# Kernel tuning notes

Measured on AMD Instinct MI355X. Metric: run time of the kernel, lower is better.

## Reference

```python
import jax, jax.numpy as jnp
import numpy as np

HIDDEN = 512
HEADS = 8


def setup_inputs() -> dict:
    key = jax.random.key(0)
    ks = jax.random.split(key, 7)
    B, S, D = 4, 2048, HIDDEN
    scale = 1.0 / np.sqrt(D)
    return {
        "src": jax.random.normal(ks[0], (B, S, D), dtype=jnp.float32),
        "Wq": jax.random.normal(ks[1], (D, D), dtype=jnp.float32) * scale,
        "bq": jax.random.normal(ks[2], (D,), dtype=jnp.float32) * 0.01,
        "Wk": jax.random.normal(ks[3], (D, D), dtype=jnp.float32) * scale,
        "bk": jax.random.normal(ks[4], (D,), dtype=jnp.float32) * 0.01,
        "Wv": jax.random.normal(ks[5], (D, D), dtype=jnp.float32) * scale,
        "bv": jax.random.normal(ks[6], (D,), dtype=jnp.float32) * 0.01,
    }


def reference(src, Wq, bq, Wk, bk, Wv, bv):
    B, S, D = src.shape
    H = HEADS
    hd = D // H
    # QKV projections -> [B, S, H, hd]
    q = (src @ Wq + bq).reshape(B, S, H, hd)
    k = (src @ Wk + bk).reshape(B, S, H, hd)
    v = (src @ Wv + bv).reshape(B, S, H, hd)
    # scores [B, H, S, S]; note: NO causal mask (matches original module)
    scores = jnp.einsum("bqhd,bkhd->bhqk", q, k) / jnp.sqrt(jnp.asarray(hd, src.dtype))
    attn = jax.nn.softmax(scores, axis=-1)
    out = jnp.einsum("bhqk,bkhd->bqhd", attn, v)
    return out.reshape(B, S, D)
```

## Files before the change

kernel.cpp:

```cpp
#include <hip/hip_runtime.h>

typedef __bf16 bf16;
typedef __bf16 bf16x8 __attribute__((ext_vector_type(8)));
typedef __bf16 bf16x4 __attribute__((ext_vector_type(4)));
typedef float f32x4 __attribute__((ext_vector_type(4)));
typedef float f32x16 __attribute__((ext_vector_type(16)));
typedef unsigned int u32;

#define QK_SCALE 0.1803368801111204f

__device__ __forceinline__ int rc16(int row, int g) {
    return row * 256 + ((g ^ (row & 15)) << 4);
}
__device__ __forceinline__ int swzb(int row, int col) {
    return (((row) << 7) + ((col) << 1)) ^ (((row) & 7) << 4);
}

__device__ __forceinline__ void gload_lds16(const void* g, void* l) {
    __builtin_amdgcn_global_load_lds(
        (const __attribute__((address_space(1))) unsigned int*)g,
        (__attribute__((address_space(3))) unsigned int*)l, 16, 0, 0);
}

__device__ __forceinline__ u32 cvtpk(float lo, float hi) {
    u32 r;
    asm("v_cvt_pk_bf16_f32 %0, %1, %2" : "=v"(r) : "v"(lo), "v"(hi));
    return r;
}
__device__ __forceinline__ void pl32swap(u32& a, u32& b) {
    asm("v_permlane32_swap_b32 %0, %1" : "+v"(a), "+v"(b));
}

__global__ __launch_bounds__(256) void cast_src(const float* __restrict__ x,
                                                bf16* __restrict__ y) {
    int i = blockIdx.x * 256 + threadIdx.x;
    float4 v = reinterpret_cast<const float4*>(x)[i];
    bf16x4 p;
    p[0] = (bf16)v.x; p[1] = (bf16)v.y; p[2] = (bf16)v.z; p[3] = (bf16)v.w;
    reinterpret_cast<bf16x4*>(y)[i] = p;
}

__global__ __launch_bounds__(256) void wtrans_all(const float* __restrict__ Wq,
                                                  const float* __restrict__ Wk,
                                                  const float* __restrict__ Wv,
                                                  bf16* __restrict__ Wt_all) {
    __shared__ float T[64][65];
    const int w = blockIdx.z;
    const float* W = w == 0 ? Wq : (w == 1 ? Wk : Wv);
    const float wsc = (w == 0) ? QK_SCALE : 1.0f;
    bf16* Wt = Wt_all + (size_t)w * 512 * 512;
    const int k0 = blockIdx.x * 64, n0 = blockIdx.y * 64;
    const int tx = threadIdx.x & 63, ty = threadIdx.x >> 6;
#pragma unroll
    for (int i = 0; i < 16; ++i) {
        int row = ty * 16 + i;
        T[row][tx] = W[(size_t)(k0 + row) * 512 + n0 + tx];
    }
    __syncthreads();
#pragma unroll
    for (int i = 0; i < 16; ++i) {
        int row = ty * 16 + i;
        Wt[(size_t)(n0 + row) * 512 + k0 + tx] = (bf16)(T[tx][row] * wsc);
    }
}

__global__ __launch_bounds__(256) void qkv_gemm_all(const bf16* __restrict__ srcb,
                                                    const bf16* __restrict__ Wt_all,
                                                    const float* __restrict__ bq,
                                                    const float* __restrict__ bk,
                                                    const float* __restrict__ bv,
                                                    bf16* __restrict__ Qb,
                                                    bf16* __restrict__ Kb,
                                                    bf16* __restrict__ Vtb) {
    __shared__ __align__(16) bf16 As[128 * 64];
    __shared__ __align__(16) bf16 Bs[128 * 64];
    const int t = threadIdx.x, lane = t & 63, wid = t >> 6;
    const int m0 = blockIdx.x * 128;
    const int n0g = blockIdx.y * 128;
    const int oi = n0g >> 9, n0 = n0g & 511;
    const float* bias = oi == 0 ? bq : (oi == 1 ? bk : bv);
    const float bsc = (oi == 0) ? QK_SCALE : 1.0f;
    bf16* outp = oi == 0 ? Qb : (oi == 1 ? Kb : Vtb);
    const bf16* Wt = Wt_all + (size_t)oi * 512 * 512;
    const bool sw = (oi == 2);
    const int wm = (wid >> 1) * 64, wn = (wid & 1) * 64;
    const int fr = lane & 15, fq = lane >> 4;

    f32x4 acc[4][4] = {};

    for (int k0 = 0; k0 < 512; k0 += 64) {
        __syncthreads();
#pragma unroll
        for (int c = 0; c < 4; ++c) {
            int u = (wid * 4 + c) * 64 + lane;
            int row = u >> 3;
            int slot = (u & 7) ^ (row & 7);
            gload_lds16(srcb + (size_t)(m0 + row) * 512 + k0 + slot * 8,
                        (char*)As + (wid * 4 + c) * 1024);
            gload_lds16(Wt + (size_t)(n0 + row) * 512 + k0 + slot * 8,
                        (char*)Bs + (wid * 4 + c) * 1024);
        }
        __syncthreads();

        bf16x8 a[2][4], b[2][4];
#pragma unroll
        for (int c = 0; c < 2; ++c)
#pragma unroll
            for (int i = 0; i < 4; ++i) {
                a[c][i] = *reinterpret_cast<const bf16x8*>(
                    (const char*)As + swzb(wm + i * 16 + fr, c * 32 + fq * 8));
                b[c][i] = *reinterpret_cast<const bf16x8*>(
                    (const char*)Bs + swzb(wn + i * 16 + fr, c * 32 + fq * 8));
            }
        if (!sw) {
#pragma unroll
            for (int i = 0; i < 4; ++i)
#pragma unroll
                for (int j = 0; j < 4; ++j)
#pragma unroll
                    for (int c = 0; c < 2; ++c)
                        acc[i][j] = __builtin_amdgcn_mfma_f32_16x16x32_bf16(a[c][i], b[c][j], acc[i][j], 0, 0, 0);
        } else {
#pragma unroll
            for (int i = 0; i < 4; ++i)
#pragma unroll
                for (int j = 0; j < 4; ++j)
#pragma unroll
                    for (int c = 0; c < 2; ++c)
                        acc[i][j] = __builtin_amdgcn_mfma_f32_16x16x32_bf16(b[c][j], a[c][i], acc[i][j], 0, 0, 0);
        }
    }

    if (!sw) {
#pragma unroll
        for (int j = 0; j < 4; ++j) {
            int n = n0 + wn + j * 16 + fr;
            float bj = bias[n] * bsc;
            int h = n >> 6, d = n & 63;
#pragma unroll
            for (int i = 0; i < 4; ++i)
#pragma unroll
                for (int r = 0; r < 4; ++r) {
                    int m = m0 + wm + i * 16 + fq * 4 + r;
                    int b_ = m >> 11, s = m & 2047;
                    outp[(((size_t)(b_ * 8 + h)) * 2048 + s) * 64 + d] =
                        (bf16)(acc[i][j][r] + bj);
                }
        }
    } else {
#pragma unroll
        for (int j = 0; j < 4; ++j)
#pragma unroll
            for (int r = 0; r < 4; ++r) {
                int n = n0 + wn + j * 16 + fq * 4 + r;
                float bj = bias[n];
                int h = n >> 6, d = n & 63;
#pragma unroll
                for (int i = 0; i < 4; ++i) {
                    int m = m0 + wm + i * 16 + fr;
                    int b_ = m >> 11, s = m & 2047;
                    outp[(((size_t)(b_ * 8 + h)) * 64 + d) * 2048 + s] =
                        (bf16)(acc[i][j][r] + bj);
                }
            }
    }
}

__global__ __launch_bounds__(512, 4) void attn_fwd(const bf16* __restrict__ Q,
                                                   const bf16* __restrict__ K,
                                                   const bf16* __restrict__ Vt,
                                                   float* __restrict__ out) {
    __shared__ __align__(16) char lds_raw[65536];
    const int t = threadIdx.x, lane = t & 63, wid = t >> 6;
    const int grp = wid >> 2, w4 = wid & 3;
    const int c31 = lane & 31, h = lane >> 5;
    const int bh = blockIdx.y;
    const int qw = blockIdx.x * 128 + w4 * 32;

    const bf16* Qp = Q + ((size_t)bh * 2048 + qw + c31) * 64;
    bf16x8 qf[4];
#pragma unroll
    for (int ks = 0; ks < 4; ++ks)
        qf[ks] = *reinterpret_cast<const bf16x8*>(&Qp[ks * 16 + h * 8]);

    bf16x8 bones;
#pragma unroll
    for (int e = 0; e < 8; ++e) bones[e] = (bf16)1.0f;

    f32x16 acc_o[2] = {};
    f32x16 acc_l = {};

    const char* Kpb0 = (const char*)(K + (size_t)bh * 2048 * 64);
    const char* Vpb0 = (const char*)(Vt + (size_t)bh * 64 * 2048);

    auto stage = [&](int buf, int tt) {
        const size_t kv0 = (size_t)(grp * 1024 + tt * 64);
        const char* Kg = Kpb0 + kv0 * 128;
        const char* Vg = Vpb0 + kv0 * 2;
        char* Kl = lds_raw + (grp * 2 + buf) * 8192;
        char* Vl = lds_raw + 32768 + (grp * 2 + buf) * 8192;
#pragma unroll
        for (int c = 0; c < 2; ++c) {
            int ch = w4 * 2 + c;
            int r = ch * 4 + (lane >> 4);
            int g = (lane & 15) ^ (r & 15);
            gload_lds16(Kg + r * 256 + g * 16, Kl + ch * 1024);
            gload_lds16(Vg + (size_t)(2 * r + (g >> 3)) * 4096 + (g & 7) * 16,
                        Vl + ch * 1024);
        }
    };

    auto compute = [&](int buf) {
        const char* Kl = lds_raw + (grp * 2 + buf) * 8192;
        const char* Vl = lds_raw + 32768 + (grp * 2 + buf) * 8192;
        const int rq = c31 >> 1, gb = (c31 & 1) * 8;

        f32x16 s0 = {}, s1 = {};
        __builtin_amdgcn_s_setprio(1);
#pragma unroll
        for (int ks = 0; ks < 4; ++ks) {
            int g = gb + ks * 2 + h;
            bf16x8 kf0 = *reinterpret_cast<const bf16x8*>(Kl + rc16(rq, g));
            s0 = __builtin_amdgcn_mfma_f32_32x32x16_bf16(kf0, qf[ks], s0, 0, 0, 0);
            bf16x8 kf1 = *reinterpret_cast<const bf16x8*>(Kl + rc16(16 + rq, g));
            s1 = __builtin_amdgcn_mfma_f32_32x32x16_bf16(kf1, qf[ks], s1, 0, 0, 0);
        }
        __builtin_amdgcn_s_setprio(0);

#pragma unroll
        for (int r = 0; r < 16; ++r) {
            s0[r] = __builtin_amdgcn_exp2f(s0[r]);
            s1[r] = __builtin_amdgcn_exp2f(s1[r]);
        }

        bf16x8 pa[4];
#pragma unroll
        for (int ktl = 0; ktl < 2; ++ktl) {
            const f32x16& sv = ktl ? s1 : s0;
#pragma unroll
            for (int k2 = 0; k2 < 2; ++k2) {
                u32 X = cvtpk(sv[8 * k2 + 0], sv[8 * k2 + 1]);
                u32 Y = cvtpk(sv[8 * k2 + 4], sv[8 * k2 + 5]);
                u32 Z = cvtpk(sv[8 * k2 + 2], sv[8 * k2 + 3]);
                u32 W = cvtpk(sv[8 * k2 + 6], sv[8 * k2 + 7]);
                pl32swap(X, Y);
                pl32swap(Z, W);
                union { bf16x8 v; u32 w[4]; } pu;
                pu.w[0] = X; pu.w[1] = Z; pu.w[2] = Y; pu.w[3] = W;
                pa[ktl * 2 + k2] = pu.v;
            }
        }

        __builtin_amdgcn_s_setprio(1);
#pragma unroll
        for (int kg = 0; kg < 4; ++kg) {
            int g = gb + kg * 2 + h;
            bf16x8 vf0 = *reinterpret_cast<const bf16x8*>(Vl + rc16(rq, g));
            acc_o[0] = __builtin_amdgcn_mfma_f32_32x32x16_bf16(pa[kg], vf0, acc_o[0], 0, 0, 0);
            bf16x8 vf1 = *reinterpret_cast<const bf16x8*>(Vl + rc16(16 + rq, g));
            acc_o[1] = __builtin_amdgcn_mfma_f32_32x32x16_bf16(pa[kg], vf1, acc_o[1], 0, 0, 0);
            acc_l = __builtin_amdgcn_mfma_f32_32x32x16_bf16(pa[kg], bones, acc_l, 0, 0, 0);
        }
        __builtin_amdgcn_s_setprio(0);
    };

    stage(0, 0);
    __syncthreads();

    for (int tt = 0; tt < 16; tt += 2) {
        stage(1, tt + 1);
        compute(0);
        __syncthreads();
        if (tt + 2 < 16) stage(0, tt + 2);
        compute(1);
        __syncthreads();
    }

    float* Os = (float*)lds_raw;
    float* Ls = (float*)(lds_raw + 32768);
    if (grp == 1) {
#pragma unroll
        for (int dt = 0; dt < 2; ++dt)
#pragma unroll
            for (int reg = 0; reg < 16; ++reg)
                Os[(((w4 * 2 + dt) * 16 + reg) * 2 + h) * 32 + c31] = acc_o[dt][reg];
#pragma unroll
        for (int reg = 0; reg < 16; ++reg)
            Ls[(w4 * 16 + reg) * 64 + lane] = acc_l[reg];
    }
    __syncthreads();
    if (grp == 0) {
        const int b_ = bh >> 3, hh = bh & 7;
#pragma unroll
        for (int reg = 0; reg < 16; ++reg) {
            float l = acc_l[reg] + Ls[(w4 * 16 + reg) * 64 + lane];
            float inv = __builtin_amdgcn_rcpf(l);
            int qr = (reg & 3) + 8 * (reg >> 2) + 4 * h;
            int s_ = qw + qr;
            size_t base = ((size_t)b_ * 2048 + s_) * 512 + hh * 64;
            out[base + c31] =
                (acc_o[0][reg] + Os[(((w4 * 2 + 0) * 16 + reg) * 2 + h) * 32 + c31]) * inv;
            out[base + 32 + c31] =
                (acc_o[1][reg] + Os[(((w4 * 2 + 1) * 16 + reg) * 2 + h) * 32 + c31]) * inv;
        }
    }
}

extern "C" void kernel_launch(void* const* d_in, const int* in_sizes, int n_in,
                              void* d_out, int out_size, void* d_ws, size_t ws_size,
                              hipStream_t stream) {
    const float* src = (const float*)d_in[0];
    const float* Wq  = (const float*)d_in[1];
    const float* bq  = (const float*)d_in[2];
    const float* Wk  = (const float*)d_in[3];
    const float* bk  = (const float*)d_in[4];
    const float* Wv  = (const float*)d_in[5];
    const float* bv  = (const float*)d_in[6];
    float* out = (float*)d_out;

    char* ws = (char*)d_ws;
    const size_t WT_SZ  = 512u * 512u * sizeof(bf16);
    const size_t QKV_SZ = 8192u * 512u * sizeof(bf16);
    bf16* WtA  = (bf16*)(ws);
    bf16* srcb = (bf16*)(ws + 3 * WT_SZ);
    bf16* Qb   = (bf16*)(ws + 3 * WT_SZ + QKV_SZ);
    bf16* Kb   = (bf16*)(ws + 3 * WT_SZ + 2 * QKV_SZ);
    bf16* Vtb  = (bf16*)(ws + 3 * WT_SZ + 3 * QKV_SZ);

    cast_src<<<4096, 256, 0, stream>>>(src, srcb);
    wtrans_all<<<dim3(8, 8, 3), 256, 0, stream>>>(Wq, Wk, Wv, WtA);

    qkv_gemm_all<<<dim3(64, 12), 256, 0, stream>>>(srcb, WtA, bq, bk, bv, Qb, Kb, Vtb);

    attn_fwd<<<dim3(16, 32), 512, 0, stream>>>(Qb, Kb, Vtb, out);
}
```

Before: 82.44 us.

## Process two 32-row query subtiles per wave to reuse K/V fragments

Each wave now handles 64 query rows instead of 32, so every K and V fragment loaded from LDS feeds two MFMAs. Block count along the query axis is halved and launch bounds drop to 2 blocks per SIMD group to allow more registers. The epilogue is reorganized so partial O and L from the second KV group are exchanged through LDS, with L placed in an extra 1 KB region. This cuts LDS traffic and K/V staging per query, at the cost of higher register pressure, lower occupancy and fewer blocks (256) to fill the GPU.

```diff
diff --git a/kernel.cpp b/kernel.cpp
--- a/kernel.cpp
+++ b/kernel.cpp
@@ -166,29 +166,34 @@
     }
 }
 
-__global__ __launch_bounds__(512, 4) void attn_fwd(const bf16* __restrict__ Q,
+__global__ __launch_bounds__(512, 2) void attn_fwd(const bf16* __restrict__ Q,
                                                    const bf16* __restrict__ K,
                                                    const bf16* __restrict__ Vt,
                                                    float* __restrict__ out) {
-    __shared__ __align__(16) char lds_raw[65536];
+    __shared__ __align__(16) char lds_raw[65536 + 1024];
     const int t = threadIdx.x, lane = t & 63, wid = t >> 6;
     const int grp = wid >> 2, w4 = wid & 3;
     const int c31 = lane & 31, h = lane >> 5;
     const int bh = blockIdx.y;
-    const int qw = blockIdx.x * 128 + w4 * 32;
-
-    const bf16* Qp = Q + ((size_t)bh * 2048 + qw + c31) * 64;
-    bf16x8 qf[4];
-#pragma unroll
-    for (int ks = 0; ks < 4; ++ks)
-        qf[ks] = *reinterpret_cast<const bf16x8*>(&Qp[ks * 16 + h * 8]);
+    const int qw = blockIdx.x * 256 + w4 * 64;
+
+    bf16x8 qf0[4], qf1[4];
+    {
+        const bf16* Qp0 = Q + ((size_t)bh * 2048 + qw + c31) * 64;
+        const bf16* Qp1 = Qp0 + 32 * 64;
+#pragma unroll
+        for (int ks = 0; ks < 4; ++ks) {
+            qf0[ks] = *reinterpret_cast<const bf16x8*>(&Qp0[ks * 16 + h * 8]);
+            qf1[ks] = *reinterpret_cast<const bf16x8*>(&Qp1[ks * 16 + h * 8]);
+        }
+    }
 
     bf16x8 bones;
 #pragma unroll
     for (int e = 0; e < 8; ++e) bones[e] = (bf16)1.0f;
 
-    f32x16 acc_o[2] = {};
-    f32x16 acc_l = {};
+    f32x16 acc_o[2][2] = {};
+    f32x16 acc_l[2] = {};
 
     const char* Kpb0 = (const char*)(K + (size_t)bh * 2048 * 64);
     const char* Vpb0 = (const char*)(Vt + (size_t)bh * 64 * 2048);
@@ -210,44 +215,52 @@
         }
     };
 
+    const int rq = c31 >> 1, gb = (c31 & 1) * 8;
+
     auto compute = [&](int buf) {
         const char* Kl = lds_raw + (grp * 2 + buf) * 8192;
         const char* Vl = lds_raw + 32768 + (grp * 2 + buf) * 8192;
-        const int rq = c31 >> 1, gb = (c31 & 1) * 8;
-
-        f32x16 s0 = {}, s1 = {};
+
+        f32x16 s00 = {}, s01 = {}, s10 = {}, s11 = {};
         __builtin_amdgcn_s_setprio(1);
 #pragma unroll
         for (int ks = 0; ks < 4; ++ks) {
             int g = gb + ks * 2 + h;
             bf16x8 kf0 = *reinterpret_cast<const bf16x8*>(Kl + rc16(rq, g));
-            s0 = __builtin_amdgcn_mfma_f32_32x32x16_bf16(kf0, qf[ks], s0, 0, 0, 0);
+            s00 = __builtin_amdgcn_mfma_f32_32x32x16_bf16(kf0, qf0[ks], s00, 0, 0, 0);
+            s10 = __builtin_amdgcn_mfma_f32_32x32x16_bf16(kf0, qf1[ks], s10, 0, 0, 0);
             bf16x8 kf1 = *reinterpret_cast<const bf16x8*>(Kl + rc16(16 + rq, g));
-            s1 = __builtin_amdgcn_mfma_f32_32x32x16_bf16(kf1, qf[ks], s1, 0, 0, 0);
+            s01 = __builtin_amdgcn_mfma_f32_32x32x16_bf16(kf1, qf0[ks], s01, 0, 0, 0);
+            s11 = __builtin_amdgcn_mfma_f32_32x32x16_bf16(kf1, qf1[ks], s11, 0, 0, 0);
         }
         __builtin_amdgcn_s_setprio(0);
 
-#pragma unroll
-        for (int r = 0; r < 16; ++r) {
-            s0[r] = __builtin_amdgcn_exp2f(s0[r]);
-            s1[r] = __builtin_amdgcn_exp2f(s1[r]);
-        }
-
-        bf16x8 pa[4];
-#pragma unroll
-        for (int ktl = 0; ktl < 2; ++ktl) {
-            const f32x16& sv = ktl ? s1 : s0;
-#pragma unroll
-            for (int k2 = 0; k2 < 2; ++k2) {
-                u32 X = cvtpk(sv[8 * k2 + 0], sv[8 * k2 + 1]);
-                u32 Y = cvtpk(sv[8 * k2 + 4], sv[8 * k2 + 5]);
-                u32 Z = cvtpk(sv[8 * k2 + 2], sv[8 * k2 + 3]);
-                u32 W = cvtpk(sv[8 * k2 + 6], sv[8 * k2 + 7]);
-                pl32swap(X, Y);
-                pl32swap(Z, W);
-                union { bf16x8 v; u32 w[4]; } pu;
-                pu.w[0] = X; pu.w[1] = Z; pu.w[2] = Y; pu.w[3] = W;
-                pa[ktl * 2 + k2] = pu.v;
+        bf16x8 pa0[4], pa1[4];
+#pragma unroll
+        for (int st = 0; st < 2; ++st) {
+            f32x16& sa = st ? s10 : s00;
+            f32x16& sb = st ? s11 : s01;
+#pragma unroll
+            for (int r = 0; r < 16; ++r) {
+                sa[r] = __builtin_amdgcn_exp2f(sa[r]);
+                sb[r] = __builtin_amdgcn_exp2f(sb[r]);
+            }
+#pragma unroll
+            for (int ktl = 0; ktl < 2; ++ktl) {
+                const f32x16& sv = ktl ? sb : sa;
+#pragma unroll
+                for (int k2 = 0; k2 < 2; ++k2) {
+                    u32 X = cvtpk(sv[8 * k2 + 0], sv[8 * k2 + 1]);
+                    u32 Y = cvtpk(sv[8 * k2 + 4], sv[8 * k2 + 5]);
+                    u32 Z = cvtpk(sv[8 * k2 + 2], sv[8 * k2 + 3]);
+                    u32 W = cvtpk(sv[8 * k2 + 6], sv[8 * k2 + 7]);
+                    pl32swap(X, Y);
+                    pl32swap(Z, W);
+                    union { bf16x8 v; u32 w[4]; } pu;
+                    pu.w[0] = X; pu.w[1] = Z; pu.w[2] = Y; pu.w[3] = W;
+                    if (st) pa1[ktl * 2 + k2] = pu.v;
+                    else    pa0[ktl * 2 + k2] = pu.v;
+                }
             }
         }
 
@@ -256,10 +269,13 @@
         for (int kg = 0; kg < 4; ++kg) {
             int g = gb + kg * 2 + h;
             bf16x8 vf0 = *reinterpret_cast<const bf16x8*>(Vl + rc16(rq, g));
-            acc_o[0] = __builtin_amdgcn_mfma_f32_32x32x16_bf16(pa[kg], vf0, acc_o[0], 0, 0, 0);
+            acc_o[0][0] = __builtin_amdgcn_mfma_f32_32x32x16_bf16(pa0[kg], vf0, acc_o[0][0], 0, 0, 0);
+            acc_o[1][0] = __builtin_amdgcn_mfma_f32_32x32x16_bf16(pa1[kg], vf0, acc_o[1][0], 0, 0, 0);
             bf16x8 vf1 = *reinterpret_cast<const bf16x8*>(Vl + rc16(16 + rq, g));
-            acc_o[1] = __builtin_amdgcn_mfma_f32_32x32x16_bf16(pa[kg], vf1, acc_o[1], 0, 0, 0);
-            acc_l = __builtin_amdgcn_mfma_f32_32x32x16_bf16(pa[kg], bones, acc_l, 0, 0, 0);
+            acc_o[0][1] = __builtin_amdgcn_mfma_f32_32x32x16_bf16(pa0[kg], vf1, acc_o[0][1], 0, 0, 0);
+            acc_o[1][1] = __builtin_amdgcn_mfma_f32_32x32x16_bf16(pa1[kg], vf1, acc_o[1][1], 0, 0, 0);
+            acc_l[0] = __builtin_amdgcn_mfma_f32_32x32x16_bf16(pa0[kg], bones, acc_l[0], 0, 0, 0);
+            acc_l[1] = __builtin_amdgcn_mfma_f32_32x32x16_bf16(pa1[kg], bones, acc_l[1], 0, 0, 0);
         }
         __builtin_amdgcn_s_setprio(0);
     };
@@ -277,32 +293,37 @@
     }
 
     float* Os = (float*)lds_raw;
-    float* Ls = (float*)(lds_raw + 32768);
+    float* Ls = (float*)(lds_raw + 65536);
     if (grp == 1) {
 #pragma unroll
-        for (int dt = 0; dt < 2; ++dt)
-#pragma unroll
-            for (int reg = 0; reg < 16; ++reg)
-                Os[(((w4 * 2 + dt) * 16 + reg) * 2 + h) * 32 + c31] = acc_o[dt][reg];
-#pragma unroll
-        for (int reg = 0; reg < 16; ++reg)
-            Ls[(w4 * 16 + reg) * 64 + lane] = acc_l[reg];
+        for (int st = 0; st < 2; ++st)
+#pragma unroll
+            for (int reg = 0; reg < 16; ++reg) {
+                int qr = (reg & 3) + 8 * (reg >> 2) + 4 * h;
+                int ql = w4 * 64 + st * 32 + qr;
+                Os[ql * 64 + c31]      = acc_o[st][0][reg];
+                Os[ql * 64 + 32 + c31] = acc_o[st][1][reg];
+                if (c31 == 0) Ls[ql] = acc_l[st][reg];
+            }
     }
     __syncthreads();
     if (grp == 0) {
         const int b_ = bh >> 3, hh = bh & 7;
 #pragma unroll
-        for (int reg = 0; reg < 16; ++reg) {
-            float l = acc_l[reg] + Ls[(w4 * 16 + reg) * 64 + lane];
-            float inv = __builtin_amdgcn_rcpf(l);
-            int qr = (reg & 3) + 8 * (reg >> 2) + 4 * h;
-            int s_ = qw + qr;
-            size_t base = ((size_t)b_ * 2048 + s_) * 512 + hh * 64;
-            out[base + c31] =
-                (acc_o[0][reg] + Os[(((w4 * 2 + 0) * 16 + reg) * 2 + h) * 32 + c31]) * inv;
-            out[base + 32 + c31] =
-                (acc_o[1][reg] + Os[(((w4 * 2 + 1) * 16 + reg) * 2 + h) * 32 + c31]) * inv;
-        }
+        for (int st = 0; st < 2; ++st)
+#pragma unroll
+            for (int reg = 0; reg < 16; ++reg) {
+                int qr = (reg & 3) + 8 * (reg >> 2) + 4 * h;
+                int ql = w4 * 64 + st * 32 + qr;
+                float l = acc_l[st][reg] + Ls[ql];
+                float inv = __builtin_amdgcn_rcpf(l);
+                int s_ = blockIdx.x * 256 + ql;
+                size_t base = ((size_t)b_ * 2048 + s_) * 512 + hh * 64;
+                out[base + c31] =
+                    (acc_o[st][0][reg] + Os[ql * 64 + c31]) * inv;
+                out[base + 32 + c31] =
+                    (acc_o[st][1][reg] + Os[ql * 64 + 32 + c31]) * inv;
+            }
     }
 }
 
@@ -332,5 +353,5 @@
 
     qkv_gemm_all<<<dim3(64, 12), 256, 0, stream>>>(srcb, WtA, bq, bk, bv, Qb, Kb, Vtb);
 
-    attn_fwd<<<dim3(16, 32), 512, 0, stream>>>(Qb, Kb, Vtb, out);
-}
+    attn_fwd<<<dim3(8, 32), 512, 0, stream>>>(Qb, Kb, Vtb, out);
+}
```

New measurement: 76.81 us. -6.8%, faster.

## Stage QKV GEMM epilogue through LDS for coalesced stores; remap attention grid

Applied to the files above, without the earlier changes.

The QKV GEMM epilogue now writes the accumulator tile into swizzled LDS and then emits 16-byte coalesced global stores for Q/K and the transposed V, replacing scattered 2-byte stores. The attention kernel switches to a 1D grid with the head index in the low bits, so consecutive blocks cover different heads' K/V. Its cross-group reduction is re-laid out, storing only one l value per row in a small extra LDS region. The extra barriers and LDS round-trip cost some time in exchange for fewer, wider store transactions.

```diff
diff --git a/kernel.cpp b/kernel.cpp
--- a/kernel.cpp
+++ b/kernel.cpp
@@ -14,6 +14,9 @@
 }
 __device__ __forceinline__ int swzb(int row, int col) {
     return (((row) << 7) + ((col) << 1)) ^ (((row) & 7) << 4);
+}
+__device__ __forceinline__ int csw(int row, int colbyte) {
+    return row * 256 + (colbyte ^ ((row & 7) << 4));
 }
 
 __device__ __forceinline__ void gload_lds16(const void* g, void* l) {
@@ -72,8 +75,9 @@
                                                     bf16* __restrict__ Qb,
                                                     bf16* __restrict__ Kb,
                                                     bf16* __restrict__ Vtb) {
-    __shared__ __align__(16) bf16 As[128 * 64];
-    __shared__ __align__(16) bf16 Bs[128 * 64];
+    __shared__ __align__(16) char gl[32768];
+    bf16* As = (bf16*)gl;
+    bf16* Bs = (bf16*)(gl + 16384);
     const int t = threadIdx.x, lane = t & 63, wid = t >> 6;
     const int m0 = blockIdx.x * 128;
     const int n0g = blockIdx.y * 128;
@@ -131,19 +135,19 @@
         }
     }
 
+    __syncthreads();
+    char* Cs = gl;
     if (!sw) {
 #pragma unroll
         for (int j = 0; j < 4; ++j) {
-            int n = n0 + wn + j * 16 + fr;
-            float bj = bias[n] * bsc;
-            int h = n >> 6, d = n & 63;
+            float bj = bias[n0 + wn + j * 16 + fr] * bsc;
 #pragma unroll
             for (int i = 0; i < 4; ++i)
 #pragma unroll
                 for (int r = 0; r < 4; ++r) {
-                    int m = m0 + wm + i * 16 + fq * 4 + r;
-                    int b_ = m >> 11, s = m & 2047;
-                    outp[(((size_t)(b_ * 8 + h)) * 2048 + s) * 64 + d] =
+                    int row = wm + i * 16 + fq * 4 + r;
+                    int colb = (wn + j * 16 + fr) * 2;
+                    *reinterpret_cast<bf16*>(Cs + csw(row, colb)) =
                         (bf16)(acc[i][j][r] + bj);
                 }
         }
@@ -152,17 +156,33 @@
         for (int j = 0; j < 4; ++j)
 #pragma unroll
             for (int r = 0; r < 4; ++r) {
-                int n = n0 + wn + j * 16 + fq * 4 + r;
-                float bj = bias[n];
-                int h = n >> 6, d = n & 63;
+                float bj = bias[n0 + wn + j * 16 + fq * 4 + r];
 #pragma unroll
                 for (int i = 0; i < 4; ++i) {
-                    int m = m0 + wm + i * 16 + fr;
-                    int b_ = m >> 11, s = m & 2047;
-                    outp[(((size_t)(b_ * 8 + h)) * 64 + d) * 2048 + s] =
+                    int row = wn + j * 16 + fq * 4 + r;
+                    int colb = (wm + i * 16 + fr) * 2;
+                    *reinterpret_cast<bf16*>(Cs + csw(row, colb)) =
                         (bf16)(acc[i][j][r] + bj);
                 }
             }
+    }
+    __syncthreads();
+
+    const int b_ = m0 >> 11, sbase = m0 & 2047, h0 = n0 >> 6;
+#pragma unroll
+    for (int it = 0; it < 8; ++it) {
+        int u = it * 256 + t;
+        int row = u >> 4, c = u & 15;
+        bf16x8 val = *reinterpret_cast<const bf16x8*>(Cs + csw(row, c * 16));
+        size_t addr;
+        if (!sw) {
+            addr = ((size_t)((b_ * 8 + h0 + (c >> 3)) * 2048 + sbase + row)) * 64
+                   + (c & 7) * 8;
+        } else {
+            addr = ((size_t)((b_ * 8 + h0 + (row >> 6)) * 64 + (row & 63))) * 2048
+                   + sbase + c * 8;
+        }
+        *reinterpret_cast<bf16x8*>(outp + addr) = val;
     }
 }
 
@@ -170,12 +190,13 @@
                                                    const bf16* __restrict__ K,
                                                    const bf16* __restrict__ Vt,
                                                    float* __restrict__ out) {
-    __shared__ __align__(16) char lds_raw[65536];
+    __shared__ __align__(16) char lds_raw[65536 + 512];
     const int t = threadIdx.x, lane = t & 63, wid = t >> 6;
     const int grp = wid >> 2, w4 = wid & 3;
     const int c31 = lane & 31, h = lane >> 5;
-    const int bh = blockIdx.y;
-    const int qw = blockIdx.x * 128 + w4 * 32;
+    const int bh = blockIdx.x & 31;
+    const int qchunk = blockIdx.x >> 5;
+    const int qw = qchunk * 128 + w4 * 32;
 
     const bf16* Qp = Q + ((size_t)bh * 2048 + qw + c31) * 64;
     bf16x8 qf[4];
@@ -210,10 +231,11 @@
         }
     };
 
+    const int rq = c31 >> 1, gb = (c31 & 1) * 8;
+
     auto compute = [&](int buf) {
         const char* Kl = lds_raw + (grp * 2 + buf) * 8192;
         const char* Vl = lds_raw + 32768 + (grp * 2 + buf) * 8192;
-        const int rq = c31 >> 1, gb = (c31 & 1) * 8;
 
         f32x16 s0 = {}, s1 = {};
         __builtin_amdgcn_s_setprio(1);
@@ -277,31 +299,30 @@
     }
 
     float* Os = (float*)lds_raw;
-    float* Ls = (float*)(lds_raw + 32768);
+    float* Ls = (float*)(lds_raw + 65536);
     if (grp == 1) {
 #pragma unroll
-        for (int dt = 0; dt < 2; ++dt)
-#pragma unroll
-            for (int reg = 0; reg < 16; ++reg)
-                Os[(((w4 * 2 + dt) * 16 + reg) * 2 + h) * 32 + c31] = acc_o[dt][reg];
-#pragma unroll
-        for (int reg = 0; reg < 16; ++reg)
-            Ls[(w4 * 16 + reg) * 64 + lane] = acc_l[reg];
+        for (int reg = 0; reg < 16; ++reg) {
+            int qr = (reg & 3) + 8 * (reg >> 2) + 4 * h;
+            int ql = w4 * 32 + qr;
+            Os[ql * 64 + c31]      = acc_o[0][reg];
+            Os[ql * 64 + 32 + c31] = acc_o[1][reg];
+            if (c31 == 0) Ls[ql] = acc_l[reg];
+        }
     }
     __syncthreads();
     if (grp == 0) {
         const int b_ = bh >> 3, hh = bh & 7;
 #pragma unroll
         for (int reg = 0; reg < 16; ++reg) {
-            float l = acc_l[reg] + Ls[(w4 * 16 + reg) * 64 + lane];
+            int qr = (reg & 3) + 8 * (reg >> 2) + 4 * h;
+            int ql = w4 * 32 + qr;
+            float l = acc_l[reg] + Ls[ql];
             float inv = __builtin_amdgcn_rcpf(l);
-            int qr = (reg & 3) + 8 * (reg >> 2) + 4 * h;
-            int s_ = qw + qr;
+            int s_ = qchunk * 128 + ql;
             size_t base = ((size_t)b_ * 2048 + s_) * 512 + hh * 64;
-            out[base + c31] =
-                (acc_o[0][reg] + Os[(((w4 * 2 + 0) * 16 + reg) * 2 + h) * 32 + c31]) * inv;
-            out[base + 32 + c31] =
-                (acc_o[1][reg] + Os[(((w4 * 2 + 1) * 16 + reg) * 2 + h) * 32 + c31]) * inv;
+            out[base + c31]      = (acc_o[0][reg] + Os[ql * 64 + c31]) * inv;
+            out[base + 32 + c31] = (acc_o[1][reg] + Os[ql * 64 + 32 + c31]) * inv;
         }
     }
 }
@@ -332,5 +353,5 @@
 
     qkv_gemm_all<<<dim3(64, 12), 256, 0, stream>>>(srcb, WtA, bq, bk, bv, Qb, Kb, Vtb);
 
-    attn_fwd<<<dim3(16, 32), 512, 0, stream>>>(Qb, Kb, Vtb, out);
-}
+    attn_fwd<<<512, 512, 0, stream>>>(Qb, Kb, Vtb, out);
+}
```

After: 81.54 us. About the same (-1.1%).
